# Kernel tuning notes

Hardware: AMD Instinct MI355X
Metric: run time of the kernel (lower is better)

Reference implementation:

```python
import jax, jax.numpy as jnp
import numpy as np

PAD_IDX = 0


def setup_inputs() -> dict:
    key = jax.random.key(0)
    ks = jax.random.split(key, 8)
    B, S, V, E, H, O = 256, 512, 50000, 300, 50, 4
    tokens = jax.random.randint(ks[0], (B, S), 0, V, dtype=jnp.int32)
    emb_table = jax.random.normal(ks[1], (V, E), dtype=jnp.float32) * 0.1
    # zero the padding row, as torch nn.Embedding(padding_idx=0) does
    emb_table = emb_table.at[PAD_IDX].set(0.0)
    s_ih = 1.0 / np.sqrt(H)
    W_ih = jax.random.uniform(ks[2], (H, E), jnp.float32, -s_ih, s_ih)
    W_hh = jax.random.uniform(ks[3], (H, H), jnp.float32, -s_ih, s_ih)
    b_ih = jax.random.uniform(ks[4], (H,), jnp.float32, -s_ih, s_ih)
    b_hh = jax.random.uniform(ks[5], (H,), jnp.float32, -s_ih, s_ih)
    s_fc = 1.0 / np.sqrt(H)
    W_fc = jax.random.uniform(ks[6], (O, H), jnp.float32, -s_fc, s_fc)
    b_fc = jax.random.uniform(ks[7], (O,), jnp.float32, -s_fc, s_fc)
    return {"tokens": tokens, "emb_table": emb_table, "W_ih": W_ih,
            "W_hh": W_hh, "b_ih": b_ih, "b_hh": b_hh,
            "W_fc": W_fc, "b_fc": b_fc}


def reference(tokens, emb_table, W_ih, W_hh, b_ih, b_hh, W_fc, b_fc):
    B, S = tokens.shape
    H = W_hh.shape[0]
    # embedding lookup; mask padding rows (grad to pad row is blocked too)
    emb = emb_table[tokens]                      # [B,S,E]
    pad_mask = (tokens != PAD_IDX)[..., None]    # [B,S,1]
    emb = jnp.where(pad_mask, emb, 0.0)
    # input projection for all timesteps at once (big GEMM)
    x_proj = jnp.einsum("bse,he->bsh", emb, W_ih) + b_ih  # [B,S,H]
    # tanh recurrence: h_t = tanh(x_t + h_{t-1} @ W_hh^T + b_hh)
    h0 = jnp.zeros((B, H), dtype=emb.dtype)

    def step(h, x_t):
        h = jnp.tanh(x_t + h @ W_hh.T + b_hh)
        return h, None

    h_last, _ = jax.lax.scan(step, h0, jnp.swapaxes(x_proj, 0, 1))  # scan over S
    # final linear head on last hidden state
    return h_last @ W_fc.T + b_fc  # [B, O]
```

## Files before the change

kernel.cpp:

```cpp
#include <hip/hip_runtime.h>
#include <hip/hip_fp16.h>

#define PTAB_STRIDE 64

typedef float    f32x4 __attribute__((ext_vector_type(4)));
typedef _Float16 half8 __attribute__((ext_vector_type(8)));
typedef _Float16 h2    __attribute__((ext_vector_type(2)));

__device__ __forceinline__ h2 u2h2(unsigned int u) {
    union { unsigned int u; h2 h; } c; c.u = u; return c.h;
}

__device__ __forceinline__ float fdot2x(h2 a, h2 b, float c) {
#if __has_builtin(__builtin_amdgcn_fdot2)
    return __builtin_amdgcn_fdot2(a, b, c, false);
#else
    return c + (float)a[0] * (float)b[0] + (float)a[1] * (float)b[1];
#endif
}

__device__ __forceinline__ float clamp9(float a) {
#if __has_builtin(__builtin_amdgcn_fmed3f)
    return __builtin_amdgcn_fmed3f(a, -9.f, 9.f);
#else
    return fminf(9.f, fmaxf(-9.f, a));
#endif
}

__global__ __launch_bounds__(64) void prep_kernel(
    const float* __restrict__ Wih, const float* __restrict__ bih,
    const float* __restrict__ bhh, __half* __restrict__ Bfrag,
    float* __restrict__ bias64)
{
    const int lane = threadIdx.x;
    const int st   = blockIdx.x;
    if (st == 40) {
        if (lane < 64) bias64[lane] = (lane < 50) ? bih[lane] + bhh[lane] : 0.f;
        return;
    }
    const int s  = st >> 2, t = st & 3;
    const int n  = 16 * t + (lane & 15);
    const int kb = lane >> 4;
    half8 v;
    #pragma unroll
    for (int j = 0; j < 8; ++j) {
        const int k = 32 * s + 8 * kb + j;
        float w = 0.f;
        if (n < 50 && k < 300) w = Wih[n * 300 + k];
        v[j] = (_Float16)w;
    }
    *reinterpret_cast<half8*>(Bfrag + ((size_t)st * 64 + lane) * 8) = v;
}

__global__ __launch_bounds__(64) void ptab_mfma(
    const float* __restrict__ emb, const __half* __restrict__ Bfrag,
    const float* __restrict__ bias64, __half* __restrict__ ptab)
{
    const int lane = threadIdx.x;
    const int v0   = blockIdx.x * 16;
    const int m    = lane & 15;
    const int kb   = lane >> 4;
    const float* Erow = emb + (size_t)(v0 + m) * 300;
    const half8* BF   = reinterpret_cast<const half8*>(Bfrag);

    f32x4 acc[4];
    #pragma unroll
    for (int t = 0; t < 4; ++t) acc[t] = (f32x4){0.f, 0.f, 0.f, 0.f};

    #pragma unroll
    for (int s = 0; s < 9; ++s) {
        const int k0 = 32 * s + 8 * kb;
        float4 p0 = *(const float4*)(Erow + k0);
        float4 p1 = *(const float4*)(Erow + k0 + 4);
        half8 a;
        a[0] = (_Float16)p0.x; a[1] = (_Float16)p0.y;
        a[2] = (_Float16)p0.z; a[3] = (_Float16)p0.w;
        a[4] = (_Float16)p1.x; a[5] = (_Float16)p1.y;
        a[6] = (_Float16)p1.z; a[7] = (_Float16)p1.w;
        #pragma unroll
        for (int t = 0; t < 4; ++t)
            acc[t] = __builtin_amdgcn_mfma_f32_16x16x32_f16(
                a, BF[(4 * s + t) * 64 + lane], acc[t], 0, 0, 0);
    }
    {
        half8 a;
        #pragma unroll
        for (int j = 0; j < 8; ++j) {
            const int k = 288 + 8 * kb + j;
            float e = 0.f;
            if (k < 300) e = Erow[k];
            a[j] = (_Float16)e;
        }
        #pragma unroll
        for (int t = 0; t < 4; ++t)
            acc[t] = __builtin_amdgcn_mfma_f32_16x16x32_f16(
                a, BF[(36 + t) * 64 + lane], acc[t], 0, 0, 0);
    }

    const int nn = lane & 15;
    #pragma unroll
    for (int t = 0; t < 4; ++t) {
        const float bt = bias64[16 * t + nn];
        #pragma unroll
        for (int r = 0; r < 4; ++r)
            ptab[(size_t)(v0 + 4 * kb + r) * PTAB_STRIDE + 16 * t + nn] =
                (__half)(acc[t][r] + bt);
    }
}

__global__ __launch_bounds__(64, 1) void rnn_kernel(
    const int* __restrict__ tokens, const __half* __restrict__ ptab,
    const float* __restrict__ Whh,
    const float* __restrict__ Wfc, const float* __restrict__ bfc,
    float* __restrict__ out)
{
    __shared__ int stok[544];
    __shared__ __align__(16) _Float16 hbuf[64];
    const int lane = threadIdx.x;
    const int b    = blockIdx.x;
    const int hc   = lane < 50 ? lane : 49;

    #pragma unroll
    for (int k = 0; k < 8; ++k)
        stok[lane + 64 * k] = tokens[b * 512 + lane + 64 * k];
    if (lane < 32) stok[512 + lane] = 0;
    __syncthreads();

    unsigned int wh_u[25];
    #pragma unroll
    for (int j = 0; j < 25; ++j) {
        float2 w2 = *(const float2*)(Whh + hc * 50 + 2 * j);
        union { h2 h; unsigned int u; } c;
        c.h = (h2){(_Float16)w2.x, (_Float16)w2.y};
        wh_u[j] = c.u;
    }

    float h = 0.f;

#define GA(T) ptab[(size_t)(T) * PTAB_STRIDE + lane]

    __half x0 = GA(stok[0]), x1 = GA(stok[1]), x2 = GA(stok[2]), x3 = GA(stok[3]);
    __half x4 = GA(stok[4]), x5 = GA(stok[5]), x6 = GA(stok[6]), x7 = GA(stok[7]);

#define SL(Q, i) __builtin_shufflevector(Q, Q, 2*(i), 2*(i)+1)
#define WH(j) u2h2(wh_u[j])

#define RNN_STEP(XV)                                                         \
    {                                                                        \
        hbuf[lane] = (_Float16)h;                \
        const half8* H8 = (const half8*)hbuf;                                \
        half8 q0 = H8[0], q1 = H8[1];                                        \
        float s0 = 0.f, s1 = 0.f, s2 = 0.f, s3 = 0.f;                        \
        s0 = fdot2x(SL(q0,0), WH(0),  s0); s1 = fdot2x(SL(q0,1), WH(1),  s1);\
        s2 = fdot2x(SL(q0,2), WH(2),  s2); s3 = fdot2x(SL(q0,3), WH(3),  s3);\
        s0 = fdot2x(SL(q1,0), WH(4),  s0); s1 = fdot2x(SL(q1,1), WH(5),  s1);\
        s2 = fdot2x(SL(q1,2), WH(6),  s2); s3 = fdot2x(SL(q1,3), WH(7),  s3);\
        half8 q2 = H8[2], q3 = H8[3];                                        \
        s0 = fdot2x(SL(q2,0), WH(8),  s0); s1 = fdot2x(SL(q2,1), WH(9),  s1);\
        s2 = fdot2x(SL(q2,2), WH(10), s2); s3 = fdot2x(SL(q2,3), WH(11), s3);\
        s0 = fdot2x(SL(q3,0), WH(12), s0); s1 = fdot2x(SL(q3,1), WH(13), s1);\
        s2 = fdot2x(SL(q3,2), WH(14), s2); s3 = fdot2x(SL(q3,3), WH(15), s3);\
        half8 q4 = H8[4], q5 = H8[5];                                        \
        h2 q6 = *(const h2*)(hbuf + 48);                                     \
        s0 = fdot2x(SL(q4,0), WH(16), s0); s1 = fdot2x(SL(q4,1), WH(17), s1);\
        s2 = fdot2x(SL(q4,2), WH(18), s2); s3 = fdot2x(SL(q4,3), WH(19), s3);\
        s0 = fdot2x(SL(q5,0), WH(20), s0); s1 = fdot2x(SL(q5,1), WH(21), s1);\
        s2 = fdot2x(SL(q5,2), WH(22), s2); s3 = fdot2x(SL(q5,3), WH(23), s3);\
        s0 = fdot2x(q6,       WH(24), s0);                                   \
        float a = ((float)(XV) + (s1 + s3)) + (s0 + s2);                     \
        a = clamp9(a);                                                       \
        float e = __expf(2.f * a);                                           \
        h = fmaf(-2.f, __builtin_amdgcn_rcpf(e + 1.f), 1.f);                 \
    }

    for (int t = 0; t < 512; t += 8) {
        __half n0 = GA(stok[t + 8]);
        __half n1 = GA(stok[t + 9]);
        __half n2 = GA(stok[t + 10]);
        __half n3 = GA(stok[t + 11]);
        __half n4 = GA(stok[t + 12]);
        __half n5 = GA(stok[t + 13]);
        __half n6 = GA(stok[t + 14]);
        __half n7 = GA(stok[t + 15]);

        RNN_STEP(x0); RNN_STEP(x1); RNN_STEP(x2); RNN_STEP(x3);
        RNN_STEP(x4); RNN_STEP(x5); RNN_STEP(x6); RNN_STEP(x7);

        x0 = n0; x1 = n1; x2 = n2; x3 = n3;
        x4 = n4; x5 = n5; x6 = n6; x7 = n7;
    }
#undef RNN_STEP
#undef SL
#undef WH
#undef GA

    float hv = (lane < 50) ? h : 0.f;
    #pragma unroll
    for (int o = 0; o < 4; ++o) {
        float w = (lane < 50) ? Wfc[o * 50 + lane] : 0.f;
        float p = hv * w;
        #pragma unroll
        for (int s = 32; s > 0; s >>= 1) p += __shfl_xor(p, s, 64);
        if (lane == 0) out[b * 4 + o] = p + bfc[o];
    }
}

extern "C" void kernel_launch(void* const* d_in, const int* in_sizes, int n_in,
                              void* d_out, int out_size, void* d_ws, size_t ws_size,
                              hipStream_t stream)
{
    const int*   tokens = (const int*)d_in[0];
    const float* emb    = (const float*)d_in[1];
    const float* Wih    = (const float*)d_in[2];
    const float* Whh    = (const float*)d_in[3];
    const float* bih    = (const float*)d_in[4];
    const float* bhh    = (const float*)d_in[5];
    const float* Wfc    = (const float*)d_in[6];
    const float* bfc    = (const float*)d_in[7];

    char* ws = (char*)d_ws;
    __half* ptab   = (__half*)ws;
    __half* Bfrag  = (__half*)(ws + 6400000);
    float*  bias64 = (float*)(ws + 6440960);
    float*  outp   = (float*)d_out;

    prep_kernel<<<41, 64, 0, stream>>>(Wih, bih, bhh, Bfrag, bias64);
    ptab_mfma<<<3125, 64, 0, stream>>>(emb, Bfrag, bias64, ptab);
    rnn_kernel<<<256, 64, 0, stream>>>(tokens, ptab, Whh, Wfc, bfc, outp);
}
```

Measured before the change: 108.2 us.

## Fold tanh exp scale into weights, prefetch embeddings, pack 4 waves per block

The constant 2*log2(e) is pre-multiplied into the projected-input table and the recurrent weights. This lets the serial tanh step use exp2 directly instead of a multiply plus exp, with the clamp widened to match. The projection kernel now software-prefetches the next embedding chunk and runs four waves per 256-thread block instead of one wave per block. Scaling before the fp16 conversion changes rounding slightly.

Result: slower. 115.4 us (+6.7%).

```diff
diff --git a/kernel.cpp b/kernel.cpp
--- a/kernel.cpp
+++ b/kernel.cpp
@@ -2,6 +2,7 @@
 #include <hip/hip_fp16.h>
 
 #define PTAB_STRIDE 64
+#define TANH_SCALE 2.885390081777927f
 
 typedef float    f32x4 __attribute__((ext_vector_type(4)));
 typedef _Float16 half8 __attribute__((ext_vector_type(8)));
@@ -19,11 +20,11 @@
 #endif
 }
 
-__device__ __forceinline__ float clamp9(float a) {
+__device__ __forceinline__ float clamp26(float a) {
 #if __has_builtin(__builtin_amdgcn_fmed3f)
-    return __builtin_amdgcn_fmed3f(a, -9.f, 9.f);
+    return __builtin_amdgcn_fmed3f(a, -26.f, 26.f);
 #else
-    return fminf(9.f, fmaxf(-9.f, a));
+    return fminf(26.f, fmaxf(-26.f, a));
 #endif
 }
 
@@ -52,37 +53,45 @@
     *reinterpret_cast<half8*>(Bfrag + ((size_t)st * 64 + lane) * 8) = v;
 }
 
-__global__ __launch_bounds__(64) void ptab_mfma(
+__global__ __launch_bounds__(256) void ptab_mfma(
     const float* __restrict__ emb, const __half* __restrict__ Bfrag,
     const float* __restrict__ bias64, __half* __restrict__ ptab)
 {
-    const int lane = threadIdx.x;
-    const int v0   = blockIdx.x * 16;
+    const int lane = threadIdx.x & 63;
+    const int wid  = threadIdx.x >> 6;
+    const int wgid = blockIdx.x * 4 + wid;
+    if (wgid >= 3125) return;
+    const int v0   = wgid * 16;
     const int m    = lane & 15;
     const int kb   = lane >> 4;
-    const float* Erow = emb + (size_t)(v0 + m) * 300;
-    const half8* BF   = reinterpret_cast<const half8*>(Bfrag);
+    const float4* E4 = (const float4*)(emb + (size_t)(v0 + m) * 300);
+    const half8* BF  = reinterpret_cast<const half8*>(Bfrag);
 
     f32x4 acc[4];
     #pragma unroll
     for (int t = 0; t < 4; ++t) acc[t] = (f32x4){0.f, 0.f, 0.f, 0.f};
 
+    float4 c0 = E4[2 * kb], c1 = E4[2 * kb + 1];
     #pragma unroll
     for (int s = 0; s < 9; ++s) {
-        const int k0 = 32 * s + 8 * kb;
-        float4 p0 = *(const float4*)(Erow + k0);
-        float4 p1 = *(const float4*)(Erow + k0 + 4);
+        float4 n0, n1;
+        if (s < 8) {
+            n0 = E4[8 * (s + 1) + 2 * kb];
+            n1 = E4[8 * (s + 1) + 2 * kb + 1];
+        }
         half8 a;
-        a[0] = (_Float16)p0.x; a[1] = (_Float16)p0.y;
-        a[2] = (_Float16)p0.z; a[3] = (_Float16)p0.w;
-        a[4] = (_Float16)p1.x; a[5] = (_Float16)p1.y;
-        a[6] = (_Float16)p1.z; a[7] = (_Float16)p1.w;
+        a[0] = (_Float16)c0.x; a[1] = (_Float16)c0.y;
+        a[2] = (_Float16)c0.z; a[3] = (_Float16)c0.w;
+        a[4] = (_Float16)c1.x; a[5] = (_Float16)c1.y;
+        a[6] = (_Float16)c1.z; a[7] = (_Float16)c1.w;
         #pragma unroll
         for (int t = 0; t < 4; ++t)
             acc[t] = __builtin_amdgcn_mfma_f32_16x16x32_f16(
                 a, BF[(4 * s + t) * 64 + lane], acc[t], 0, 0, 0);
+        if (s < 8) { c0 = n0; c1 = n1; }
     }
     {
+        const float* Erow = (const float*)E4;
         half8 a;
         #pragma unroll
         for (int j = 0; j < 8; ++j) {
@@ -104,7 +113,7 @@
         #pragma unroll
         for (int r = 0; r < 4; ++r)
             ptab[(size_t)(v0 + 4 * kb + r) * PTAB_STRIDE + 16 * t + nn] =
-                (__half)(acc[t][r] + bt);
+                (__half)((acc[t][r] + bt) * TANH_SCALE);
     }
 }
 
@@ -131,7 +140,7 @@
     for (int j = 0; j < 25; ++j) {
         float2 w2 = *(const float2*)(Whh + hc * 50 + 2 * j);
         union { h2 h; unsigned int u; } c;
-        c.h = (h2){(_Float16)w2.x, (_Float16)w2.y};
+        c.h = (h2){(_Float16)(w2.x * TANH_SCALE), (_Float16)(w2.y * TANH_SCALE)};
         wh_u[j] = c.u;
     }
 
@@ -168,8 +177,8 @@
         s2 = fdot2x(SL(q5,2), WH(22), s2); s3 = fdot2x(SL(q5,3), WH(23), s3);\
         s0 = fdot2x(q6,       WH(24), s0);                                   \
         float a = ((float)(XV) + (s1 + s3)) + (s0 + s2);                     \
-        a = clamp9(a);                                                       \
-        float e = __expf(2.f * a);                                           \
+        a = clamp26(a);                                                      \
+        float e = exp2f(a);                       \
         h = fmaf(-2.f, __builtin_amdgcn_rcpf(e + 1.f), 1.f);                 \
     }
 
@@ -225,6 +234,6 @@
     float*  outp   = (float*)d_out;
 
     prep_kernel<<<41, 64, 0, stream>>>(Wih, bih, bhh, Bfrag, bias64);
-    ptab_mfma<<<3125, 64, 0, stream>>>(emb, Bfrag, bias64, ptab);
+    ptab_mfma<<<782, 256, 0, stream>>>(emb, Bfrag, bias64, ptab);
     rnn_kernel<<<256, 64, 0, stream>>>(tokens, ptab, Whh, Wfc, bfc, outp);
 }
```
